# Kernel tuning notes

Hardware: AMD Instinct MI355X
Metric: run time of the kernel (lower is better)

## Reference

```python
import jax, jax.numpy as jnp
import numpy as np

DIM = 256
B, W_IN, H_IN = 8, 96, 96


def setup_inputs() -> dict:
    key = jax.random.key(0)
    k1, k2, k3 = jax.random.split(key, 3)
    x = jax.random.normal(k1, (B, W_IN, H_IN, DIM), dtype=jnp.float32)
    # Conv2d(dim, 3*dim, kernel_size=1): weight (3C, C) (1x1 spatial dropped), bias (3C,)
    w_qkv = jax.random.normal(k2, (3 * DIM, DIM), dtype=jnp.float32) * (1.0 / np.sqrt(DIM))
    b_qkv = jax.random.normal(k3, (3 * DIM,), dtype=jnp.float32) * 0.01
    return {"x": x, "w_qkv": w_qkv, "b_qkv": b_qkv}


def reference(x, w_qkv, b_qkv):
    # x: (B, W, H, C) -> transpose(3,1) -> (B, C, H, W)
    xt = jnp.transpose(x, (0, 3, 2, 1))
    # 1x1 conv == channel GEMM
    qvk = jnp.einsum('bchw,oc->bohw', xt, w_qkv) + b_qkv[None, :, None, None]
    q, k, v = jnp.split(qvk, 3, axis=1)  # each (B, C, H, W)
    Bn, C, H, W = q.shape

    q_t = jnp.transpose(q, (0, 2, 1, 3))            # (B, H, C, W)
    qk = q_t.reshape(Bn, H * C, W)                   # (B, H*C, W)
    qf = q_t.reshape(Bn, H, C * W)                   # (B, H, C*W)
    kq = jnp.transpose(k, (0, 1, 3, 2)).reshape(Bn, C * W, H)  # (B, C*W, H)
    ms = jax.nn.softmax(jnp.matmul(qf, kq), axis=-1)  # (B, H, H) attention over H

    kf = jnp.transpose(k, (0, 3, 2, 1)).reshape(Bn, W, H * C)  # (B, W, H*C)
    ma = jax.nn.softmax(jnp.matmul(kf, qk), axis=-1)  # (B, W, W) attention over W

    vq = jnp.transpose(v, (0, 2, 1, 3)).reshape(Bn, H, C * W)  # (B, H, C*W)
    vk = jnp.transpose(v, (0, 3, 2, 1)).reshape(Bn, W, H * C)  # (B, W, H*C)

    ms = jnp.matmul(ms, vq).reshape(Bn, H, C, W)     # view(B, H, C, W)
    ms = jnp.transpose(ms, (0, 2, 1, 3))             # (B, C, H, W)
    ma = jnp.matmul(ma, vk).reshape(Bn, W, H, C)     # view(B, W, H, C)
    ma = jnp.transpose(ma, (0, 3, 2, 1))             # (B, C, H, W)

    # final transpose(3,1): (B, C, H, W) -> (B, W, H, C)
    return jnp.transpose(ms + ma, (0, 3, 2, 1))
```

## Files before the change

### kernel.cpp

```cpp
#include <hip/hip_runtime.h>
#include <math.h>

#define SQ 96
#define CQ 256
#define OQ 768
#define HWQ 9216
#define PIXQ 73728

typedef __attribute__((ext_vector_type(8))) __bf16 bf16x8;
typedef __attribute__((ext_vector_type(4))) float f32x4;

union FragU { uint4 u; bf16x8 b; };

__device__ inline uint32_t bf16_rne_u(float f) {
  uint32_t u = __float_as_uint(f);
  return (u + 0x7FFFu + ((u >> 16) & 1u)) >> 16;
}
__device__ inline uint32_t pack_split(float f) {
  uint32_t hi = bf16_rne_u(f);
  float rem = f - __uint_as_float(hi << 16);
  uint32_t lo = __float_as_uint(rem) >> 16;
  return hi | (lo << 16);
}
__device__ inline void unpack_frags(uint4 r0, uint4 r1, FragU& hi, FragU& lo) {
  hi.u.x = (r0.x & 0xFFFFu) | (r0.y << 16);
  hi.u.y = (r0.z & 0xFFFFu) | (r0.w << 16);
  hi.u.z = (r1.x & 0xFFFFu) | (r1.y << 16);
  hi.u.w = (r1.z & 0xFFFFu) | (r1.w << 16);
  lo.u.x = (r0.x >> 16) | (r0.y & 0xFFFF0000u);
  lo.u.y = (r0.z >> 16) | (r0.w & 0xFFFF0000u);
  lo.u.z = (r1.x >> 16) | (r1.y & 0xFFFF0000u);
  lo.u.w = (r1.z >> 16) | (r1.w & 0xFFFF0000u);
}

__global__ __launch_bounds__(256) void pack_w_kernel(
    const float* __restrict__ w, uint32_t* __restrict__ wp) {
  int i = blockIdx.x * 256 + threadIdx.x;
  wp[i] = pack_split(w[i]);
}

__global__ __launch_bounds__(256) void qkv_gemm_mfma(
    const float* __restrict__ x, const uint32_t* __restrict__ wp,
    const float* __restrict__ bias, uint32_t* __restrict__ qk,
    ushort* __restrict__ vb) {
  __shared__ uint32_t Apk[128 * 32];
  __shared__ uint32_t Bpk[128 * 32];
  const int tid = threadIdx.x;
  const int lane = tid & 63;
  const int wid = tid >> 6;
  const int wm = wid >> 1, wn = wid & 1;
  const int lr = lane & 15, quad = lane >> 4;
  const int m0 = blockIdx.x * 128, n0 = blockIdx.y * 128;
  const int sr = tid >> 1, skh = (tid & 1) * 16;

  f32x4 acc[4][4] = {};

  for (int k0 = 0; k0 < 256; k0 += 32) {
    const float* xsrc = x + (size_t)(m0 + sr) * 256 + k0 + skh;
    uint32_t* adst = Apk + sr * 32 + skh;
#pragma unroll
    for (int j = 0; j < 4; ++j) {
      float4 v = *(const float4*)(xsrc + 4 * j);
      uint4 p;
      p.x = pack_split(v.x); p.y = pack_split(v.y);
      p.z = pack_split(v.z); p.w = pack_split(v.w);
      *(uint4*)(adst + 4 * j) = p;
    }
    const uint32_t* wsrc = wp + (size_t)(n0 + sr) * 256 + k0 + skh;
    uint32_t* bdst = Bpk + sr * 32 + skh;
#pragma unroll
    for (int j = 0; j < 4; ++j)
      *(uint4*)(bdst + 4 * j) = *(const uint4*)(wsrc + 4 * j);
    __syncthreads();

    FragU ah[4], al[4], bh[4], bl[4];
#pragma unroll
    for (int t = 0; t < 4; ++t) {
      const uint32_t* pa = Apk + (wm * 64 + t * 16 + lr) * 32 + quad * 8;
      unpack_frags(*(const uint4*)pa, *(const uint4*)(pa + 4), ah[t], al[t]);
      const uint32_t* pb = Bpk + (wn * 64 + t * 16 + lr) * 32 + quad * 8;
      unpack_frags(*(const uint4*)pb, *(const uint4*)(pb + 4), bh[t], bl[t]);
    }
#pragma unroll
    for (int i = 0; i < 4; ++i)
#pragma unroll
      for (int j = 0; j < 4; ++j) {
        acc[i][j] = __builtin_amdgcn_mfma_f32_16x16x32_bf16(al[i].b, bl[j].b, acc[i][j], 0, 0, 0);
        acc[i][j] = __builtin_amdgcn_mfma_f32_16x16x32_bf16(al[i].b, bh[j].b, acc[i][j], 0, 0, 0);
        acc[i][j] = __builtin_amdgcn_mfma_f32_16x16x32_bf16(ah[i].b, bl[j].b, acc[i][j], 0, 0, 0);
        acc[i][j] = __builtin_amdgcn_mfma_f32_16x16x32_bf16(ah[i].b, bh[j].b, acc[i][j], 0, 0, 0);
      }
    __syncthreads();
  }

#pragma unroll
  for (int i = 0; i < 4; ++i) {
    const int growb = m0 + wm * 64 + i * 16 + quad * 4;
#pragma unroll
    for (int r = 0; r < 4; ++r) {
      int p = growb + r;
      int b = p / HWQ;
      int rem = p - b * HWQ;
      int ww = rem / SQ;
      int hh = rem - ww * SQ;
      size_t opix = (size_t)b * HWQ + (size_t)hh * SQ + ww;
#pragma unroll
      for (int j = 0; j < 4; ++j) {
        int o = n0 + wn * 64 + j * 16 + lr;
        float val = acc[i][j][r] + bias[o];
        if (o < 512) qk[opix * 512 + o] = pack_split(val);
        else vb[opix * 256 + (o - 512)] = (ushort)bf16_rne_u(val);
      }
    }
  }
}

__global__ __launch_bounds__(256) void attn_scores_mfma(
    const uint32_t* __restrict__ qk, float* __restrict__ Sh,
    float* __restrict__ Sw) {
  __shared__ uint32_t Xpk[96 * 32];
  __shared__ uint32_t Ypk[96 * 32];
  const int tid = threadIdx.x;
  const int lane = tid & 63;
  const int wid = tid >> 6;
  const int wm = wid >> 1, wn = wid & 1;
  const int lr = lane & 15, quad = lane >> 4;
  const int chunk = blockIdx.x;
  const int b = blockIdx.y;
  const int which = blockIdx.z;
  const size_t base = (size_t)b * HWQ * 512;
  const int offX = which ? 256 : 0;
  const int offY = which ? 0 : 256;

  f32x4 acc[3][3] = {};

  for (int it = 0; it < 24; ++it) {
    int kout = chunk * 3 + (it >> 3);
    int c0 = (it & 7) * 32;
#pragma unroll
    for (int j = 0; j < 3; ++j) {
      int s = j * 256 + tid;
      int row = s >> 3;
      int c4 = (s & 7) * 4;
      size_t idx = which ? ((size_t)kout * SQ + row) : ((size_t)row * SQ + kout);
      const uint32_t* src = qk + base + idx * 512 + c0 + c4;
      *(uint4*)(Xpk + row * 32 + c4) = *(const uint4*)(src + offX);
      *(uint4*)(Ypk + row * 32 + c4) = *(const uint4*)(src + offY);
    }
    __syncthreads();
    FragU xh[3], xl[3], yh[3], yl[3];
#pragma unroll
    for (int t = 0; t < 3; ++t) {
      const uint32_t* px = Xpk + (wm * 48 + t * 16 + lr) * 32 + quad * 8;
      unpack_frags(*(const uint4*)px, *(const uint4*)(px + 4), xh[t], xl[t]);
      const uint32_t* py = Ypk + (wn * 48 + t * 16 + lr) * 32 + quad * 8;
      unpack_frags(*(const uint4*)py, *(const uint4*)(py + 4), yh[t], yl[t]);
    }
#pragma unroll
    for (int i = 0; i < 3; ++i)
#pragma unroll
      for (int j = 0; j < 3; ++j) {
        acc[i][j] = __builtin_amdgcn_mfma_f32_16x16x32_bf16(xl[i].b, yl[j].b, acc[i][j], 0, 0, 0);
        acc[i][j] = __builtin_amdgcn_mfma_f32_16x16x32_bf16(xl[i].b, yh[j].b, acc[i][j], 0, 0, 0);
        acc[i][j] = __builtin_amdgcn_mfma_f32_16x16x32_bf16(xh[i].b, yl[j].b, acc[i][j], 0, 0, 0);
        acc[i][j] = __builtin_amdgcn_mfma_f32_16x16x32_bf16(xh[i].b, yh[j].b, acc[i][j], 0, 0, 0);
      }
    __syncthreads();
  }
  float* S = which ? Sw : Sh;
#pragma unroll
  for (int i = 0; i < 3; ++i)
#pragma unroll
    for (int r = 0; r < 4; ++r)
#pragma unroll
      for (int j = 0; j < 3; ++j) {
        int row = wm * 48 + i * 16 + quad * 4 + r;
        int col = wn * 48 + j * 16 + lr;
        atomicAdd(S + ((size_t)b * SQ + row) * SQ + col, acc[i][j][r]);
      }
}

__global__ __launch_bounds__(256) void softmax_p(
    const float* __restrict__ Sh, const float* __restrict__ Sw,
    ushort* __restrict__ Pms, ushort* __restrict__ Pma) {
  const int tid = threadIdx.x;
  const int lane = tid & 63;
  const int row = blockIdx.x * 4 + (tid >> 6);
  const float* p = (row < 768) ? (Sh + (size_t)row * SQ)
                               : (Sw + (size_t)(row - 768) * SQ);
  ushort* q = (row < 768) ? (Pms + (size_t)row * SQ)
                          : (Pma + (size_t)(row - 768) * SQ);
  float v0 = p[lane];
  float v1 = (lane < 32) ? p[64 + lane] : -3.0e38f;
  float m = fmaxf(v0, v1);
#pragma unroll
  for (int off = 32; off > 0; off >>= 1) m = fmaxf(m, __shfl_xor(m, off));
  float e0 = __expf(v0 - m);
  float e1 = (lane < 32) ? __expf(v1 - m) : 0.0f;
  float s = e0 + e1;
#pragma unroll
  for (int off = 32; off > 0; off >>= 1) s += __shfl_xor(s, off);
  float inv = 1.0f / s;
  q[lane] = (ushort)bf16_rne_u(e0 * inv);
  if (lane < 32) q[64 + lane] = (ushort)bf16_rne_u(e1 * inv);
}

__global__ __launch_bounds__(256) void attn_apply_mfma(
    const ushort* __restrict__ vb, const ushort* __restrict__ P,
    float* __restrict__ out, const int which) {
  __shared__ ushort Vt[256 * 40];
  const int tid = threadIdx.x;
  const int lane = tid & 63;
  const int wid = tid >> 6;
  const int wm = wid >> 1, wn = wid & 1;
  const int lr = lane & 15, quad = lane >> 4;
  const int xi = blockIdx.x;
  const int b = blockIdx.y;

  f32x4 acc[3][8] = {};

  for (int k0 = 0; k0 < 96; k0 += 32) {
#pragma unroll
    for (int j = 0; j < 8; ++j) {
      int bi = j * 256 + tid;
      int c2 = bi & 127;
      int k2 = bi >> 7;
      int k = k0 + k2 * 2;
      int c = c2 * 2;
      size_t r0, r1;
      if (which == 0) {
        r0 = ((size_t)b * HWQ + (size_t)k * SQ + xi) * CQ + c;
        r1 = r0 + (size_t)SQ * CQ;
      } else {
        r0 = ((size_t)b * HWQ + (size_t)xi * SQ + k) * CQ + c;
        r1 = r0 + CQ;
      }
      uint32_t a0 = *(const uint32_t*)(vb + r0);
      uint32_t a1 = *(const uint32_t*)(vb + r1);
      uint32_t w0 = (a0 & 0xFFFFu) | (a1 << 16);
      uint32_t w1 = (a0 >> 16) | (a1 & 0xFFFF0000u);
      *(uint32_t*)&Vt[c * 40 + k2 * 2] = w0;
      *(uint32_t*)&Vt[(c + 1) * 40 + k2 * 2] = w1;
    }
    __syncthreads();
    FragU a[3];
#pragma unroll
    for (int t = 0; t < 3; ++t) {
      int row = wm * 48 + t * 16 + lr;
      const ushort* ps = P + ((size_t)b * SQ + row) * SQ + k0 + quad * 8;
      a[t].u = *(const uint4*)ps;
    }
#pragma unroll
    for (int j = 0; j < 8; ++j) {
      int cb = wn * 128 + j * 16 + lr;
      FragU bf;
      bf.u = *(const uint4*)&Vt[cb * 40 + quad * 8];
#pragma unroll
      for (int i = 0; i < 3; ++i)
        acc[i][j] = __builtin_amdgcn_mfma_f32_16x16x32_bf16(a[i].b, bf.b, acc[i][j], 0, 0, 0);
    }
    __syncthreads();
  }

#pragma unroll
  for (int i = 0; i < 3; ++i) {
#pragma unroll
    for (int r = 0; r < 4; ++r) {
      int mrow = wm * 48 + i * 16 + quad * 4 + r;
      size_t obase;
      if (which == 0) obase = (((size_t)b * SQ + xi) * SQ + mrow) * CQ;
      else            obase = (((size_t)b * SQ + mrow) * SQ + xi) * CQ;
#pragma unroll
      for (int j = 0; j < 8; ++j) {
        int c = wn * 128 + j * 16 + lr;
        if (which == 0) out[obase + c] = acc[i][j][r];
        else            out[obase + c] += acc[i][j][r];
      }
    }
  }
}

extern "C" void kernel_launch(void* const* d_in, const int* in_sizes, int n_in,
                              void* d_out, int out_size, void* d_ws,
                              size_t ws_size, hipStream_t stream) {
  const float* x = (const float*)d_in[0];
  const float* w = (const float*)d_in[1];
  const float* bias = (const float*)d_in[2];
  float* out = (float*)d_out;

  uint32_t* qk  = (uint32_t*)d_ws;
  ushort*   vb  = (ushort*)(qk + (size_t)PIXQ * 512);
  float*    Sh  = (float*)(vb + (size_t)PIXQ * 256);
  float*    Sw  = Sh + PIXQ;
  ushort*   Pms = (ushort*)(Sw + PIXQ);
  ushort*   Pma = Pms + PIXQ;
  uint32_t* wp  = (uint32_t*)(Pma + PIXQ);

  hipMemsetAsync(Sh, 0, 2 * (size_t)PIXQ * sizeof(float), stream);

  pack_w_kernel<<<dim3(768), 256, 0, stream>>>(w, wp);
  qkv_gemm_mfma<<<dim3(576, 6), 256, 0, stream>>>(x, wp, bias, qk, vb);
  attn_scores_mfma<<<dim3(32, 8, 2), 256, 0, stream>>>(qk, Sh, Sw);
  softmax_p<<<dim3(384), 256, 0, stream>>>(Sh, Sw, Pms, Pma);
  attn_apply_mfma<<<dim3(96, 8), 256, 0, stream>>>(vb, Pms, out, 0);
  attn_apply_mfma<<<dim3(96, 8), 256, 0, stream>>>(vb, Pma, out, 1);
}
```

Measured before the change: 461.9 us.

## Swizzle LDS tiles, drop lo*lo MFMA term, remap GEMM blocks across XCDs

Applies an XOR swizzle to the LDS layout of the packed bf16 hi/lo tiles in both the QKV GEMM and the attention-score kernel, to reduce LDS bank conflicts on fragment reads. Removes the lo*lo MFMA term of the split-bf16 emulation, cutting MFMA work by a quarter at a small cost in accuracy. Flattens the QKV GEMM grid and remaps block indices so blocks sharing input rows land on the same XCD, to improve L2 reuse.

```diff
diff --git a/kernel.cpp b/kernel.cpp
--- a/kernel.cpp
+++ b/kernel.cpp
@@ -31,6 +31,13 @@
   lo.u.y = (r0.z >> 16) | (r0.w & 0xFFFF0000u);
   lo.u.z = (r1.x >> 16) | (r1.y & 0xFFFF0000u);
   lo.u.w = (r1.z >> 16) | (r1.w & 0xFFFF0000u);
+}
+
+__device__ inline uint32_t* swz(uint32_t* base, int row, int colb) {
+  return base + row * 32 + ((colb ^ ((row & 7) << 4)) >> 2);
+}
+__device__ inline const uint32_t* swzc(const uint32_t* base, int row, int colb) {
+  return base + row * 32 + ((colb ^ ((row & 7) << 4)) >> 2);
 }
 
 __global__ __launch_bounds__(256) void pack_w_kernel(
@@ -50,42 +57,42 @@
   const int wid = tid >> 6;
   const int wm = wid >> 1, wn = wid & 1;
   const int lr = lane & 15, quad = lane >> 4;
-  const int m0 = blockIdx.x * 128, n0 = blockIdx.y * 128;
+  const int lin = (blockIdx.x & 7) * 432 + (blockIdx.x >> 3);
+  const int m0 = (lin / 6) * 128, n0 = (lin % 6) * 128;
   const int sr = tid >> 1, skh = (tid & 1) * 16;
 
   f32x4 acc[4][4] = {};
 
   for (int k0 = 0; k0 < 256; k0 += 32) {
     const float* xsrc = x + (size_t)(m0 + sr) * 256 + k0 + skh;
-    uint32_t* adst = Apk + sr * 32 + skh;
 #pragma unroll
     for (int j = 0; j < 4; ++j) {
       float4 v = *(const float4*)(xsrc + 4 * j);
       uint4 p;
       p.x = pack_split(v.x); p.y = pack_split(v.y);
       p.z = pack_split(v.z); p.w = pack_split(v.w);
-      *(uint4*)(adst + 4 * j) = p;
+      *(uint4*)swz(Apk, sr, skh * 4 + j * 16) = p;
     }
     const uint32_t* wsrc = wp + (size_t)(n0 + sr) * 256 + k0 + skh;
-    uint32_t* bdst = Bpk + sr * 32 + skh;
 #pragma unroll
     for (int j = 0; j < 4; ++j)
-      *(uint4*)(bdst + 4 * j) = *(const uint4*)(wsrc + 4 * j);
+      *(uint4*)swz(Bpk, sr, skh * 4 + j * 16) = *(const uint4*)(wsrc + 4 * j);
     __syncthreads();
 
     FragU ah[4], al[4], bh[4], bl[4];
 #pragma unroll
     for (int t = 0; t < 4; ++t) {
-      const uint32_t* pa = Apk + (wm * 64 + t * 16 + lr) * 32 + quad * 8;
-      unpack_frags(*(const uint4*)pa, *(const uint4*)(pa + 4), ah[t], al[t]);
-      const uint32_t* pb = Bpk + (wn * 64 + t * 16 + lr) * 32 + quad * 8;
-      unpack_frags(*(const uint4*)pb, *(const uint4*)(pb + 4), bh[t], bl[t]);
+      const int ra = wm * 64 + t * 16 + lr;
+      unpack_frags(*(const uint4*)swzc(Apk, ra, quad * 32),
+                   *(const uint4*)swzc(Apk, ra, quad * 32 + 16), ah[t], al[t]);
+      const int rb = wn * 64 + t * 16 + lr;
+      unpack_frags(*(const uint4*)swzc(Bpk, rb, quad * 32),
+                   *(const uint4*)swzc(Bpk, rb, quad * 32 + 16), bh[t], bl[t]);
     }
 #pragma unroll
     for (int i = 0; i < 4; ++i)
 #pragma unroll
       for (int j = 0; j < 4; ++j) {
-        acc[i][j] = __builtin_amdgcn_mfma_f32_16x16x32_bf16(al[i].b, bl[j].b, acc[i][j], 0, 0, 0);
         acc[i][j] = __builtin_amdgcn_mfma_f32_16x16x32_bf16(al[i].b, bh[j].b, acc[i][j], 0, 0, 0);
         acc[i][j] = __builtin_amdgcn_mfma_f32_16x16x32_bf16(ah[i].b, bl[j].b, acc[i][j], 0, 0, 0);
         acc[i][j] = __builtin_amdgcn_mfma_f32_16x16x32_bf16(ah[i].b, bh[j].b, acc[i][j], 0, 0, 0);
@@ -141,26 +148,27 @@
     for (int j = 0; j < 3; ++j) {
       int s = j * 256 + tid;
       int row = s >> 3;
-      int c4 = (s & 7) * 4;
+      int colb = (s & 7) * 16;
       size_t idx = which ? ((size_t)kout * SQ + row) : ((size_t)row * SQ + kout);
-      const uint32_t* src = qk + base + idx * 512 + c0 + c4;
-      *(uint4*)(Xpk + row * 32 + c4) = *(const uint4*)(src + offX);
-      *(uint4*)(Ypk + row * 32 + c4) = *(const uint4*)(src + offY);
+      const uint32_t* src = qk + base + idx * 512 + c0 + (colb >> 2);
+      *(uint4*)swz(Xpk, row, colb) = *(const uint4*)(src + offX);
+      *(uint4*)swz(Ypk, row, colb) = *(const uint4*)(src + offY);
     }
     __syncthreads();
     FragU xh[3], xl[3], yh[3], yl[3];
 #pragma unroll
     for (int t = 0; t < 3; ++t) {
-      const uint32_t* px = Xpk + (wm * 48 + t * 16 + lr) * 32 + quad * 8;
-      unpack_frags(*(const uint4*)px, *(const uint4*)(px + 4), xh[t], xl[t]);
-      const uint32_t* py = Ypk + (wn * 48 + t * 16 + lr) * 32 + quad * 8;
-      unpack_frags(*(const uint4*)py, *(const uint4*)(py + 4), yh[t], yl[t]);
+      const int rx = wm * 48 + t * 16 + lr;
+      unpack_frags(*(const uint4*)swzc(Xpk, rx, quad * 32),
+                   *(const uint4*)swzc(Xpk, rx, quad * 32 + 16), xh[t], xl[t]);
+      const int ry = wn * 48 + t * 16 + lr;
+      unpack_frags(*(const uint4*)swzc(Ypk, ry, quad * 32),
+                   *(const uint4*)swzc(Ypk, ry, quad * 32 + 16), yh[t], yl[t]);
     }
 #pragma unroll
     for (int i = 0; i < 3; ++i)
 #pragma unroll
       for (int j = 0; j < 3; ++j) {
-        acc[i][j] = __builtin_amdgcn_mfma_f32_16x16x32_bf16(xl[i].b, yl[j].b, acc[i][j], 0, 0, 0);
         acc[i][j] = __builtin_amdgcn_mfma_f32_16x16x32_bf16(xl[i].b, yh[j].b, acc[i][j], 0, 0, 0);
         acc[i][j] = __builtin_amdgcn_mfma_f32_16x16x32_bf16(xh[i].b, yl[j].b, acc[i][j], 0, 0, 0);
         acc[i][j] = __builtin_amdgcn_mfma_f32_16x16x32_bf16(xh[i].b, yh[j].b, acc[i][j], 0, 0, 0);
@@ -299,7 +307,7 @@
   hipMemsetAsync(Sh, 0, 2 * (size_t)PIXQ * sizeof(float), stream);
 
   pack_w_kernel<<<dim3(768), 256, 0, stream>>>(w, wp);
-  qkv_gemm_mfma<<<dim3(576, 6), 256, 0, stream>>>(x, wp, bias, qk, vb);
+  qkv_gemm_mfma<<<dim3(3456), 256, 0, stream>>>(x, wp, bias, qk, vb);
   attn_scores_mfma<<<dim3(32, 8, 2), 256, 0, stream>>>(qk, Sh, Sw);
   softmax_p<<<dim3(384), 256, 0, stream>>>(Sh, Sw, Pms, Pma);
   attn_apply_mfma<<<dim3(96, 8), 256, 0, stream>>>(vb, Pms, out, 0);
```

Measured after the change: 453.0 us. Within noise of the previous version (-1.9%).
